# Kernel tuning notes

Measured on AMD Instinct MI355X. Metric: run time of the kernel, lower is better.

Reference implementation:

```python
import jax, jax.numpy as jnp
import numpy as np

HEADS = 6
EPS = 1e-5


def _na_idx(L, k, d):
    # NATTEN-style dilated neighborhood: work within dilation cosets,
    # clamp window to stay inside the image (window shifts at borders).
    i = np.arange(L)
    g = i % d
    p = i // d
    Lg = (L - g + d - 1) // d  # coset length per position
    start = np.clip(p - k // 2, 0, Lg - k)
    j = np.arange(k)
    nbr = g[:, None] + d * (start[:, None] + j[None, :])          # [L,k] neighbor coords
    rel = (start[:, None] + j[None, :]) - p[:, None] + (k - 1)    # [L,k] rpb index in [0,2k-2]
    return jnp.asarray(nbr, jnp.int32), jnp.asarray(rel, jnp.int32)


def _na2d(x, qkv_w, qkv_b, proj_w, proj_b, rpb, heads, k, d):
    # x: [B,H,W,C] NHWC neighborhood attention with relative positional bias
    B, H, W, C = x.shape
    dh = C // heads
    scale = dh ** -0.5
    qkv = (x @ qkv_w + qkv_b).reshape(B, H, W, 3, heads, dh)
    qkv = jnp.transpose(qkv, (3, 0, 4, 1, 2, 5))  # [3,B,h,H,W,dh]
    q, kk, v = qkv[0] * scale, qkv[1], qkv[2]
    nh, rh = _na_idx(H, k, d)
    nw, rw = _na_idx(W, k, d)

    def gather(t):  # [B,h,H,W,dh] -> [B,h,H,W,k,k,dh]
        t = t[:, :, nh]              # [B,h,H,k,W,dh]
        t = t[:, :, :, :, nw]        # [B,h,H,k,W,k,dh]
        return jnp.transpose(t, (0, 1, 2, 4, 3, 5, 6))

    kn, vn = gather(kk), gather(v)
    attn = jnp.einsum('bhxyd,bhxyijd->bhxyij', q, kn)  # [B,h,H,W,k,k]
    bias = rpb[:, rh]                  # [h,H,k,2k-1]
    bias = bias[:, :, :, rw]           # [h,H,k,W,k]
    bias = jnp.transpose(bias, (0, 1, 3, 2, 4))  # [h,H,W,k,k]
    attn = attn + bias[None]
    attn = jax.nn.softmax(attn.reshape(B, heads, H, W, k * k), axis=-1)
    attn = attn.reshape(B, heads, H, W, k, k)
    out = jnp.einsum('bhxyij,bhxyijd->bhxyd', attn, vn)
    out = jnp.transpose(out, (0, 2, 3, 1, 4)).reshape(B, H, W, C)
    return out @ proj_w + proj_b


def _rln(x, w, b, m1_w, m1_b, m2_w, m2_b):
    # Revised LayerNorm: normalize over (C,H,W) per sample; meta1/meta2 are 1x1 convs on std/mean
    mean = jnp.mean(x, axis=(1, 2, 3), keepdims=True)
    std = jnp.sqrt(jnp.mean((x - mean) ** 2, axis=(1, 2, 3), keepdims=True) + EPS)
    out = (x - mean) / std * w + b
    rescale = m1_w[None, :, None, None] * std + m1_b[None, :, None, None]
    rebias = m2_w[None, :, None, None] * mean + m2_b[None, :, None, None]
    return out, rescale, rebias


def _c11(x, w, b):  # 1x1 conv on NCHW == per-pixel linear
    return jnp.einsum('bchw,oc->bohw', x, w) + b[None, :, None, None]


def _gelu(x):
    return jax.nn.gelu(x, approximate=False)


def reference(x, ln_w, ln_b, m1_w, m1_b, m2_w, m2_b, qkv1_w, qkv1_b, proj1_w, proj1_b, rpb1, qkv2_w, qkv2_b, proj2_w, proj2_b, rpb2, mlp_w1, mlp_b1, mlp_w2, mlp_b2, bn_g, bn_b, bn_m, bn_v, pa_w1, pa_b1, pa_w2, pa_b2, ca_w1, ca_b1, ca_w2, ca_b2, m2a_w1, m2a_b1, m2a_w2, m2a_b2):
    # ---- NA block 1 (kernel 7, dilation 1) ----
    sc = x
    y, rs, rb = _rln(x, ln_w, ln_b, m1_w, m1_b, m2_w, m2_b)
    a = _na2d(jnp.transpose(y, (0, 2, 3, 1)), qkv1_w, qkv1_b, proj1_w, proj1_b, rpb1, HEADS, 7, 1)
    x = sc + jnp.transpose(a, (0, 3, 1, 2)) * rs + rb
    # ---- NA block 2 (kernel 5, dilation 8) ----
    sc = x
    y, rs, rb = _rln(x, ln_w, ln_b, m1_w, m1_b, m2_w, m2_b)
    a = _na2d(jnp.transpose(y, (0, 2, 3, 1)), qkv2_w, qkv2_b, proj2_w, proj2_b, rpb2, HEADS, 5, 8)
    x = sc + jnp.transpose(a, (0, 3, 1, 2)) * rs + rb
    # ---- MLP (source reuses the pre-attn2 shortcut `sc`) ----
    y, rs, rb = _rln(x, ln_w, ln_b, m1_w, m1_b, m2_w, m2_b)
    m = _c11(jax.nn.relu(_c11(y, mlp_w1, mlp_b1)), mlp_w2, mlp_b2)
    x = sc + m * rs + rb
    # ---- BN + pixel attention + channel attention + mlp2 ----
    sc = x
    inv = jax.lax.rsqrt(bn_v + EPS)
    y = (x - bn_m[None, :, None, None]) * (inv * bn_g)[None, :, None, None] + bn_b[None, :, None, None]
    pa = jax.nn.sigmoid(_c11(_gelu(_c11(y, pa_w1, pa_b1)), pa_w2, pa_b2))  # [B,1,H,W]
    y = pa * y
    gap = jnp.mean(y, axis=(2, 3), keepdims=True)
    ca = jax.nn.sigmoid(_c11(_gelu(_c11(gap, ca_w1, ca_b1)), ca_w2, ca_b2))  # [B,C,1,1]
    y = ca * y
    y = _c11(_gelu(_c11(y, m2a_w1, m2a_b1)), m2a_w2, m2a_b2)
    return sc + y


def setup_inputs() -> dict:
    key = jax.random.key(0)
    B, C, H, W, HID = 4, 96, 64, 64, 384
    ks = iter(jax.random.split(key, 48))

    def rn(shape, s=0.02):
        return jax.random.normal(next(ks), shape, jnp.float32) * s

    d = {}
    d['x'] = jax.random.normal(next(ks), (B, C, H, W), jnp.float32)
    d['ln_w'] = jnp.ones((1, C, 1, 1), jnp.float32)
    d['ln_b'] = jnp.zeros((1, C, 1, 1), jnp.float32)
    d['m1_w'] = rn((C,)); d['m1_b'] = jnp.ones((C,), jnp.float32)
    d['m2_w'] = rn((C,)); d['m2_b'] = jnp.zeros((C,), jnp.float32)
    d['qkv1_w'] = rn((C, 3 * C)); d['qkv1_b'] = jnp.zeros((3 * C,), jnp.float32)
    d['proj1_w'] = rn((C, C)); d['proj1_b'] = jnp.zeros((C,), jnp.float32)
    d['rpb1'] = rn((HEADS, 13, 13))
    d['qkv2_w'] = rn((C, 3 * C)); d['qkv2_b'] = jnp.zeros((3 * C,), jnp.float32)
    d['proj2_w'] = rn((C, C)); d['proj2_b'] = jnp.zeros((C,), jnp.float32)
    d['rpb2'] = rn((HEADS, 9, 9))
    d['mlp_w1'] = rn((HID, C)); d['mlp_b1'] = jnp.zeros((HID,), jnp.float32)
    d['mlp_w2'] = rn((C, HID)); d['mlp_b2'] = jnp.zeros((C,), jnp.float32)
    d['bn_g'] = jnp.ones((C,), jnp.float32); d['bn_b'] = jnp.zeros((C,), jnp.float32)
    d['bn_m'] = jnp.zeros((C,), jnp.float32); d['bn_v'] = jnp.ones((C,), jnp.float32)
    d['pa_w1'] = rn((C // 8, C)); d['pa_b1'] = jnp.zeros((C // 8,), jnp.float32)
    d['pa_w2'] = rn((1, C // 8)); d['pa_b2'] = jnp.zeros((1,), jnp.float32)
    d['ca_w1'] = rn((C, C)); d['ca_b1'] = jnp.zeros((C,), jnp.float32)
    d['ca_w2'] = rn((C, C)); d['ca_b2'] = jnp.zeros((C,), jnp.float32)
    d['m2a_w1'] = rn((C, C)); d['m2a_b1'] = jnp.zeros((C,), jnp.float32)
    d['m2a_w2'] = rn((C, C)); d['m2a_b2'] = jnp.zeros((C,), jnp.float32)
    return d
```

## Files before the change

### kernel.cpp

```cpp
#include <hip/hip_runtime.h>
#include <math.h>

#define CC 96
#define NP 4096
#define NHEADS 6
#define NELEMF 393216.0f
#define EPSF 1e-5f

typedef __attribute__((ext_vector_type(8))) short bf16x8;
typedef __attribute__((ext_vector_type(4))) float f32x4;
#define MFMA16(a,b,c) __builtin_amdgcn_mfma_f32_16x16x32_bf16(a,b,c,0,0,0)

#define WQKV1  64
#define WQKV2  (WQKV1+13824)
#define WPROJ1 (WQKV2+13824)
#define WPROJ2 (WPROJ1+4608)
#define WMLP1  (WPROJ2+4608)
#define WMLP2  (WMLP1+18432)
#define WM2A1  (WMLP2+18432)
#define WM2A2  (WM2A1+4608)
#define WPA1T  (WM2A2+4608)
#define WBNS   (WPA1T+1152)
#define WCA1T  (WBNS+192)
#define WCA2T  (WCA1T+9216)
#define WS_Q   870784
#define WS_K   (WS_Q+786432)
#define WS_V   (WS_K+786432)
#define WS_ATTPM (WS_V+786432)
#define WS_X1  (WS_ATTPM+786432)
#define WS_X2  (WS_X1+1572864)
#define WS_X3  (WS_X2+1572864)
#define WS_PA  (WS_X3+1572864)
#define WS_GAP (WS_PA+16384)

__device__ __forceinline__ float gelu_f(float x){
  return 0.5f * x * (1.0f + erff(x * 0.7071067811865476f));
}
__device__ __forceinline__ float sigmoid_f(float x){
  return 1.0f / (1.0f + __expf(-x));
}
__device__ __forceinline__ unsigned short bfr(float f){
  unsigned int u = __float_as_uint(f);
  u += 0x7fffu + ((u >> 16) & 1u);
  return (unsigned short)(u >> 16);
}
__device__ __forceinline__ float bflo16(unsigned short u){ return __uint_as_float(((unsigned int)u) << 16); }
__device__ __forceinline__ float bflo(unsigned int u){ return __uint_as_float(u << 16); }
__device__ __forceinline__ float bfhi(unsigned int u){ return __uint_as_float(u & 0xffff0000u); }
__device__ __forceinline__ void get_ms(const float* st, int b, float& mean, float& inv, float& stdv){
  float s = st[b], s2 = st[4+b];
  mean = s * (1.0f/NELEMF);
  float var = fmaxf(s2 * (1.0f/NELEMF) - mean*mean, 0.0f);
  stdv = sqrtf(var + EPSF);
  inv = 1.0f / stdv;
}
__device__ __forceinline__ float ldf(const float* p, int i){ return p[i]; }
__device__ __forceinline__ float ldf(const unsigned short* p, int i){ return bflo16(p[i]); }
__device__ __forceinline__ void load4(const float* p, float4& v){ v = *(const float4*)p; }
__device__ __forceinline__ void load4(const unsigned short* p, float4& v){
  ushort4 u = *(const ushort4*)p;
  v.x = bflo16(u.x); v.y = bflo16(u.y); v.z = bflo16(u.z); v.w = bflo16(u.w);
}

__device__ __forceinline__ float dotg(const float* qv, const uint4* p){
  uint4 a = p[0], b = p[1];
  float s;
  s  = qv[0]*bflo(a.x);            s = fmaf(qv[1],  bfhi(a.x), s);
  s = fmaf(qv[2],  bflo(a.y), s);  s = fmaf(qv[3],  bfhi(a.y), s);
  s = fmaf(qv[4],  bflo(a.z), s);  s = fmaf(qv[5],  bfhi(a.z), s);
  s = fmaf(qv[6],  bflo(a.w), s);  s = fmaf(qv[7],  bfhi(a.w), s);
  s = fmaf(qv[8],  bflo(b.x), s);  s = fmaf(qv[9],  bfhi(b.x), s);
  s = fmaf(qv[10], bflo(b.y), s);  s = fmaf(qv[11], bfhi(b.y), s);
  s = fmaf(qv[12], bflo(b.z), s);  s = fmaf(qv[13], bfhi(b.z), s);
  s = fmaf(qv[14], bflo(b.w), s);  s = fmaf(qv[15], bfhi(b.w), s);
  return s;
}
__device__ __forceinline__ void pvg(float w, const uint4* p, float* acc){
  uint4 a = p[0], b = p[1];
  acc[0]  = fmaf(w, bflo(a.x), acc[0]);  acc[1]  = fmaf(w, bfhi(a.x), acc[1]);
  acc[2]  = fmaf(w, bflo(a.y), acc[2]);  acc[3]  = fmaf(w, bfhi(a.y), acc[3]);
  acc[4]  = fmaf(w, bflo(a.z), acc[4]);  acc[5]  = fmaf(w, bfhi(a.z), acc[5]);
  acc[6]  = fmaf(w, bflo(a.w), acc[6]);  acc[7]  = fmaf(w, bfhi(a.w), acc[7]);
  acc[8]  = fmaf(w, bflo(b.x), acc[8]);  acc[9]  = fmaf(w, bfhi(b.x), acc[9]);
  acc[10] = fmaf(w, bflo(b.y), acc[10]); acc[11] = fmaf(w, bfhi(b.y), acc[11]);
  acc[12] = fmaf(w, bflo(b.z), acc[12]); acc[13] = fmaf(w, bfhi(b.z), acc[13]);
  acc[14] = fmaf(w, bflo(b.w), acc[14]); acc[15] = fmaf(w, bfhi(b.w), acc[15]);
}

__global__ void prep_stats_kernel(const float* __restrict__ x, float* __restrict__ st,
                             const float* __restrict__ q1, const float* __restrict__ q2,
                             const float* __restrict__ p1, const float* __restrict__ p2,
                             const float* __restrict__ w1, const float* __restrict__ w2,
                             const float* __restrict__ a1, const float* __restrict__ a2,
                             const float* __restrict__ pw1,
                             const float* __restrict__ bg, const float* __restrict__ bb,
                             const float* __restrict__ bm, const float* __restrict__ bv,
                             const float* __restrict__ cw1, const float* __restrict__ cw2,
                             float* __restrict__ ws){
  if(blockIdx.x < 384){
    int b = blockIdx.x / CC, c = blockIdx.x % CC;
    const float4* p4 = (const float4*)(x + (size_t)(b*CC + c)*NP);
    float s = 0.f, s2 = 0.f;
    for(int i = threadIdx.x; i < 1024; i += 256){
      float4 v = p4[i];
      s += v.x + v.y + v.z + v.w;
      s2 = fmaf(v.x, v.x, fmaf(v.y, v.y, fmaf(v.z, v.z, fmaf(v.w, v.w, s2))));
    }
    for(int off = 32; off > 0; off >>= 1){ s += __shfl_down(s, off); s2 += __shfl_down(s2, off); }
    __shared__ float ls[8];
    int wid = threadIdx.x >> 6;
    if((threadIdx.x & 63) == 0){ ls[wid] = s; ls[4+wid] = s2; }
    __syncthreads();
    if(threadIdx.x == 0){
      atomicAdd(&st[b],   ls[0]+ls[1]+ls[2]+ls[3]);
      atomicAdd(&st[4+b], ls[4]+ls[5]+ls[6]+ls[7]);
    }
    return;
  }
  int gid = (blockIdx.x - 384)*256 + threadIdx.x;
  if(gid < 27648){ int n = gid/96, c = gid%96; ((unsigned short*)(ws+WQKV1))[gid] = bfr(q1[c*288+n]); }
  else if(gid < 55296){ int g = gid-27648; int n = g/96, c = g%96; ((unsigned short*)(ws+WQKV2))[g] = bfr(q2[c*288+n]); }
  else if(gid < 64512){ int g = gid-55296; int n = g/96, c = g%96; ((unsigned short*)(ws+WPROJ1))[g] = bfr(p1[c*96+n]); }
  else if(gid < 73728){ int g = gid-64512; int n = g/96, c = g%96; ((unsigned short*)(ws+WPROJ2))[g] = bfr(p2[c*96+n]); }
  else if(gid < 110592){ int g = gid-73728; ((unsigned short*)(ws+WMLP1))[g] = bfr(w1[g]); }
  else if(gid < 147456){ int g = gid-110592; ((unsigned short*)(ws+WMLP2))[g] = bfr(w2[g]); }
  else if(gid < 156672){ int g = gid-147456; ((unsigned short*)(ws+WM2A1))[g] = bfr(a1[g]); }
  else if(gid < 165888){ int g = gid-156672; ((unsigned short*)(ws+WM2A2))[g] = bfr(a2[g]); }
  else if(gid < 167040){ int g = gid-165888; int c = g/12, h = g%12; ws[WPA1T + g] = pw1[h*96+c]; }
  else if(gid < 167136){ int c = gid-167040;
    float sc = rsqrtf(bv[c] + EPSF) * bg[c];
    ws[WBNS + c] = sc;
    ws[WBNS + 96 + c] = bb[c] - bm[c]*sc;
  }
  else if(gid < 167520){ ws[WS_GAP + (gid-167136)] = 0.f; }
  else if(gid < 176736){ int g = gid-167520; int o = g/96, c = g%96; ws[WCA1T + c*96 + o] = cw1[g]; }
  else if(gid < 185952){ int g = gid-176736; int o = g/96, c = g%96; ws[WCA2T + c*96 + o] = cw2[g]; }
}

template<typename AT>
__global__ void __launch_bounds__(512) gemm_qkv_kernel(
    const AT* __restrict__ xin, const float* __restrict__ st,
    const float* __restrict__ lnw, const float* __restrict__ lnb,
    const unsigned short* __restrict__ wT, const float* __restrict__ qb,
    unsigned short* __restrict__ qo, unsigned short* __restrict__ ko, unsigned short* __restrict__ vo){
  __shared__ unsigned short Atl[64*104];
  __shared__ float scl[96], ofs[96];
  int m_base = blockIdx.x*64;
  int b = m_base >> 12, pxl0 = m_base & 4095;
  float mean, inv, stdv; get_ms(st, b, mean, inv, stdv);
  int tid = threadIdx.x;
  if(tid < 96){ float s = inv*lnw[tid]; scl[tid] = s; ofs[tid] = lnb[tid] - mean*s; }
  __syncthreads();
  const AT* src = xin + (size_t)b*CC*NP + pxl0;
  for(int idx = tid; idx < 96*16; idx += 512){
    int c = idx >> 4, p4 = (idx & 15) << 2;
    float4 v; load4(src + (size_t)c*NP + p4, v);
    float s = scl[c], o = ofs[c];
    Atl[(p4+0)*104 + c] = bfr(fmaf(v.x, s, o));
    Atl[(p4+1)*104 + c] = bfr(fmaf(v.y, s, o));
    Atl[(p4+2)*104 + c] = bfr(fmaf(v.z, s, o));
    Atl[(p4+3)*104 + c] = bfr(fmaf(v.w, s, o));
  }
  __syncthreads();
  int w = tid >> 6, lane = tid & 63, ml = lane & 15, q = lane >> 4;
  int row = w & 3, nh = w >> 2;
  const unsigned short* arow = Atl + (row*16 + ml)*104;
  bf16x8 av[3];
  #pragma unroll
  for(int ks = 0; ks < 3; ++ks) av[ks] = *(const bf16x8*)(arow + ks*32 + q*8);
  f32x4 z = {0.f,0.f,0.f,0.f};
  #pragma unroll
  for(int g0 = 0; g0 < 3; ++g0){
    int g = nh*3 + g0;
    f32x4 acc[3] = {z, z, z};
    #pragma unroll
    for(int ks = 0; ks < 3; ++ks){
      #pragma unroll
      for(int gg = 0; gg < 3; ++gg){
        bf16x8 bv = *(const bf16x8*)(wT + (g*48 + gg*16 + ml)*96 + ks*32 + q*8);
        acc[gg] = MFMA16(av[ks], bv, acc[gg]);
      }
    }
    #pragma unroll
    for(int gg = 0; gg < 3; ++gg){
      int nfb = g*48 + gg*16;
      int t = nfb/96, head = (nfb%96) >> 4;
      float scale = (t == 0) ? 0.25f : 1.0f;
      unsigned short* dst = (t == 0) ? qo : (t == 1) ? ko : vo;
      float bias = qb[nfb + ml];
      #pragma unroll
      for(int r = 0; r < 4; ++r){
        int pxl = pxl0 + row*16 + q*4 + r;
        dst[(((size_t)(b*NHEADS + head))*NP + pxl)*16 + ml] = bfr((acc[gg][r] + bias)*scale);
      }
    }
  }
}

template<int K, int D, int RPB, typename SCT>
__global__ void __launch_bounds__(512) attnproj_kernel(
    const unsigned short* __restrict__ qb, const unsigned short* __restrict__ kb,
    const unsigned short* __restrict__ vb, const float* __restrict__ rpb,
    const unsigned short* __restrict__ wT, const float* __restrict__ pb,
    const SCT* __restrict__ scx, const float* __restrict__ st,
    const float* __restrict__ m1w, const float* __restrict__ m1b,
    const float* __restrict__ m2w, const float* __restrict__ m2b,
    unsigned short* __restrict__ dst, float* __restrict__ st_out){
  __shared__ __align__(16) char smbuf[26624];
  __shared__ float rpbl[NHEADS*RPB*RPB];
  __shared__ float ls[16];
  unsigned short* attout = (unsigned short*)smbuf;
  float* T = (float*)smbuf;
  int b = blockIdx.x >> 6;
  int x = blockIdx.x & 63;
  int tid = threadIdx.x;
  for(int i = tid; i < NHEADS*RPB*RPB; i += 512) rpbl[i] = rpb[i];
  __syncthreads();

  if(tid < 384){
    int head = tid >> 6;
    int y = tid & 63;
    int bh = b*NHEADS + head;
    int gx = (D == 1) ? 0 : (x & (D-1));
    int px = (D == 1) ? x : (x >> 3);
    int Lgx = (64 - gx + D - 1) / D;
    int sx = min(max(px - K/2, 0), Lgx - K);
    int gy = (D == 1) ? 0 : (y & (D-1));
    int py = (D == 1) ? y : (y >> 3);
    int Lgy = (64 - gy + D - 1) / D;
    int sy = min(max(py - K/2, 0), Lgy - K);
    int dxb = sx - px + (K-1);
    int dyb = sy - py + (K-1);
    int pix = x*64 + y;

    float qv[16];
    {
      const uint4* qg = (const uint4*)(qb + ((size_t)bh*NP + pix)*16);
      uint4 qa = qg[0], qb4 = qg[1];
      qv[0]=bflo(qa.x);  qv[1]=bfhi(qa.x);  qv[2]=bflo(qa.y);  qv[3]=bfhi(qa.y);
      qv[4]=bflo(qa.z);  qv[5]=bfhi(qa.z);  qv[6]=bflo(qa.w);  qv[7]=bfhi(qa.w);
      qv[8]=bflo(qb4.x); qv[9]=bfhi(qb4.x); qv[10]=bflo(qb4.y);qv[11]=bfhi(qb4.y);
      qv[12]=bflo(qb4.z);qv[13]=bfhi(qb4.z);qv[14]=bflo(qb4.w);qv[15]=bfhi(qb4.w);
    }
    const unsigned short* kgb = kb + (size_t)bh*NP*16;
    const unsigned short* vgb = vb + (size_t)bh*NP*16;

    float sc[K*K];
    #pragma unroll
    for(int i = 0; i < K; ++i){
      int colx = gx + D*(sx + i);
      const unsigned short* kcol = kgb + (size_t)colx*64*16;
      const float* br = rpbl + (head*RPB + (i + dxb))*RPB + dyb;
      #pragma unroll
      for(int j = 0; j < K; ++j){
        int wwy = gy + D*(sy + j);
        sc[i*K + j] = dotg(qv, (const uint4*)(kcol + wwy*16)) + br[j];
      }
    }
    float mx = -1e30f;
    #pragma unroll
    for(int n = 0; n < K*K; ++n) mx = fmaxf(mx, sc[n]);
    float sum = 0.f;
    #pragma unroll
    for(int n = 0; n < K*K; ++n){ float e = __expf(sc[n] - mx); sc[n] = e; sum += e; }
    float rs = 1.0f / sum;
    float acc[16];
    #pragma unroll
    for(int d = 0; d < 16; ++d) acc[d] = 0.f;
    #pragma unroll
    for(int i = 0; i < K; ++i){
      int colx = gx + D*(sx + i);
      const unsigned short* vcol = vgb + (size_t)colx*64*16;
      #pragma unroll
      for(int j = 0; j < K; ++j){
        int wwy = gy + D*(sy + j);
        pvg(sc[i*K + j] * rs, (const uint4*)(vcol + wwy*16), acc);
      }
    }
    unsigned int ow[8];
    #pragma unroll
    for(int p = 0; p < 8; ++p)
      ow[p] = (unsigned int)bfr(acc[2*p]) | ((unsigned int)bfr(acc[2*p+1]) << 16);
    unsigned short* op = attout + y*104 + head*16;
    *(uint4*)op = make_uint4(ow[0], ow[1], ow[2], ow[3]);
    *(uint4*)(op + 8) = make_uint4(ow[4], ow[5], ow[6], ow[7]);
  }
  __syncthreads();

  int w = tid >> 6, lane = tid & 63, ml = lane & 15, q = lane >> 4;
  int row = w & 3, nh = w >> 2;
  f32x4 z = {0.f,0.f,0.f,0.f};
  f32x4 acc[3] = {z, z, z};
  {
    const unsigned short* arow = attout + (row*16 + ml)*104;
    #pragma unroll
    for(int ks = 0; ks < 3; ++ks){
      bf16x8 av = *(const bf16x8*)(arow + ks*32 + q*8);
      #pragma unroll
      for(int g0 = 0; g0 < 3; ++g0){
        int g = nh*3 + g0;
        bf16x8 bv = *(const bf16x8*)(wT + (g*16 + ml)*96 + ks*32 + q*8);
        acc[g0] = MFMA16(av, bv, acc[g0]);
      }
    }
  }
  __syncthreads();
  #pragma unroll
  for(int g0 = 0; g0 < 3; ++g0){
    int g = nh*3 + g0;
    #pragma unroll
    for(int r = 0; r < 4; ++r)
      T[(g*16 + ml)*68 + row*16 + q*4 + r] = acc[g0][r];
  }
  __syncthreads();
  int pxl0 = x*64;
  float mean, inv, stdv; get_ms(st, b, mean, inv, stdv);
  float s = 0.f, s2 = 0.f;
  for(int idx = tid; idx < 96*64; idx += 512){
    int n = idx >> 6, p = idx & 63;
    float rsf = fmaf(m1w[n], stdv, m1b[n]);
    float rbf = fmaf(m2w[n], mean, m2b[n]);
    int ad = (b*CC + n)*NP + pxl0 + p;
    float val = ldf(scx, ad) + (T[n*68 + p] + pb[n])*rsf + rbf;
    dst[ad] = bfr(val);
    s += val; s2 = fmaf(val, val, s2);
  }
  for(int off = 32; off > 0; off >>= 1){ s += __shfl_down(s, off); s2 += __shfl_down(s2, off); }
  if(lane == 0){ ls[w] = s; ls[8+w] = s2; }
  __syncthreads();
  if(tid == 0){
    float a0 = 0.f, a1 = 0.f;
    #pragma unroll
    for(int i = 0; i < 8; ++i){ a0 += ls[i]; a1 += ls[8+i]; }
    atomicAdd(&st_out[b], a0);
    atomicAdd(&st_out[4+b], a1);
  }
}

__global__ void __launch_bounds__(512) gemm_mlp_kernel(
    const unsigned short* __restrict__ xin, const float* __restrict__ st,
    const float* __restrict__ lnw, const float* __restrict__ lnb,
    const unsigned short* __restrict__ w1T, const float* __restrict__ b1,
    const unsigned short* __restrict__ w2T, const float* __restrict__ b2,
    const unsigned short* __restrict__ scx,
    const float* __restrict__ m1w, const float* __restrict__ m1b,
    const float* __restrict__ m2w, const float* __restrict__ m2b,
    float* __restrict__ dst,
    const float* __restrict__ bns, const float* __restrict__ pw1t,
    const float* __restrict__ pb1, const float* __restrict__ pw2,
    const float* __restrict__ pb2, float* __restrict__ pa,
    float* __restrict__ gap){
  __shared__ __align__(16) char smbuf[63488];
  __shared__ float scl[96], ofs[96];
  unsigned short* Atl  = (unsigned short*)smbuf;
  unsigned short* hidL = (unsigned short*)(smbuf + 13312);
  float* T = (float*)(smbuf + 13312);
  float* gpart = (float*)smbuf;
  int m_base = blockIdx.x*64;
  int b = m_base >> 12, pxl0 = m_base & 4095;
  float mean, inv, stdv; get_ms(st, b, mean, inv, stdv);
  int tid = threadIdx.x;
  if(tid < 96){ float s = inv*lnw[tid]; scl[tid] = s; ofs[tid] = lnb[tid] - mean*s; }
  __syncthreads();
  const unsigned short* src = xin + (size_t)b*CC*NP + pxl0;
  for(int idx = tid; idx < 96*16; idx += 512){
    int c = idx >> 4, p4 = (idx & 15) << 2;
    float4 v; load4(src + (size_t)c*NP + p4, v);
    float s = scl[c], o = ofs[c];
    Atl[(p4+0)*104 + c] = bfr(fmaf(v.x, s, o));
    Atl[(p4+1)*104 + c] = bfr(fmaf(v.y, s, o));
    Atl[(p4+2)*104 + c] = bfr(fmaf(v.z, s, o));
    Atl[(p4+3)*104 + c] = bfr(fmaf(v.w, s, o));
  }
  __syncthreads();
  int w = tid >> 6, lane = tid & 63, ml = lane & 15, q = lane >> 4;
  int row = w & 3, nh = w >> 2;
  f32x4 z = {0.f,0.f,0.f,0.f};
  {
    const unsigned short* arow = Atl + (row*16 + ml)*104;
    bf16x8 av[3];
    #pragma unroll
    for(int ks = 0; ks < 3; ++ks) av[ks] = *(const bf16x8*)(arow + ks*32 + q*8);
    #pragma unroll
    for(int g0 = 0; g0 < 4; ++g0){
      int g = nh*4 + g0;
      f32x4 acc[3] = {z, z, z};
      #pragma unroll
      for(int ks = 0; ks < 3; ++ks){
        #pragma unroll
        for(int gg = 0; gg < 3; ++gg){
          bf16x8 bv = *(const bf16x8*)(w1T + (g*48 + gg*16 + ml)*96 + ks*32 + q*8);
          acc[gg] = MFMA16(av[ks], bv, acc[gg]);
        }
      }
      #pragma unroll
      for(int gg = 0; gg < 3; ++gg){
        int n = g*48 + gg*16 + ml;
        float bias = b1[n];
        #pragma unroll
        for(int r = 0; r < 4; ++r)
          hidL[(row*16 + q*4 + r)*392 + n] = bfr(fmaxf(acc[gg][r] + bias, 0.f));
      }
    }
  }
  __syncthreads();
  f32x4 acc2[3] = {z, z, z};
  {
    const unsigned short* arow = hidL + (row*16 + ml)*392;
    #pragma unroll
    for(int ks = 0; ks < 12; ++ks){
      bf16x8 av = *(const bf16x8*)(arow + ks*32 + q*8);
      #pragma unroll
      for(int g0 = 0; g0 < 3; ++g0){
        int g = nh*3 + g0;
        bf16x8 bv = *(const bf16x8*)(w2T + (g*16 + ml)*384 + ks*32 + q*8);
        acc2[g0] = MFMA16(av, bv, acc2[g0]);
      }
    }
  }
  __syncthreads();
  #pragma unroll
  for(int g0 = 0; g0 < 3; ++g0){
    int g = nh*3 + g0;
    #pragma unroll
    for(int r = 0; r < 4; ++r)
      T[(g*16 + ml)*68 + row*16 + q*4 + r] = acc2[g0][r];
  }
  __syncthreads();
  for(int idx = tid; idx < 96*64; idx += 512){
    int n = idx >> 6, px = idx & 63;
    float rsf = fmaf(m1w[n], stdv, m1b[n]);
    float rbf = fmaf(m2w[n], mean, m2b[n]);
    int ad = (b*CC + n)*NP + pxl0 + px;
    float val = ldf(scx, ad) + (T[n*68 + px] + b2[n])*rsf + rbf;
    dst[ad] = val;
    T[n*68 + px] = val;
  }
  __syncthreads();
  int pxq = tid >> 3, t = tid & 7;
  float yvv[12], acc[12];
  #pragma unroll
  for(int h = 0; h < 12; ++h) acc[h] = 0.f;
  #pragma unroll 6
  for(int cc = 0; cc < 12; ++cc){
    int c = t*12 + cc;
    float yv = fmaf(T[c*68 + pxq], bns[c], bns[96 + c]);
    yvv[cc] = yv;
    #pragma unroll
    for(int h = 0; h < 12; ++h) acc[h] = fmaf(yv, pw1t[c*12 + h], acc[h]);
  }
  #pragma unroll
  for(int h = 0; h < 12; ++h){
    acc[h] += __shfl_xor(acc[h], 1);
    acc[h] += __shfl_xor(acc[h], 2);
    acc[h] += __shfl_xor(acc[h], 4);
  }
  float s = pb2[0];
  #pragma unroll
  for(int h = 0; h < 12; ++h) s = fmaf(gelu_f(acc[h] + pb1[h]), pw2[h], s);
  float pav = sigmoid_f(s);
  if(t == 0) pa[b*NP + pxl0 + pxq] = pav;
  #pragma unroll 6
  for(int cc = 0; cc < 12; ++cc){
    float g = yvv[cc] * pav;
    g += __shfl_xor(g, 8);  g += __shfl_xor(g, 16); g += __shfl_xor(g, 32);
    if(lane < 8) gpart[w*96 + lane*12 + cc] = g;
  }
  __syncthreads();
  if(tid < 96){
    int c = tid;
    float v = 0.f;
    #pragma unroll
    for(int ww = 0; ww < 8; ++ww) v += gpart[ww*96 + c];
    atomicAdd(&gap[b*96 + c], v * (1.0f/4096.0f));
  }
}

__global__ void __launch_bounds__(512) gemm_m2a_kernel(
    const float* __restrict__ x3, const float* __restrict__ bns,
    const float* __restrict__ pa, const float* __restrict__ gap,
    const float* __restrict__ cw1T, const float* __restrict__ cb1,
    const float* __restrict__ cw2T, const float* __restrict__ cb2,
    const unsigned short* __restrict__ w1T, const float* __restrict__ b1,
    const unsigned short* __restrict__ w2T, const float* __restrict__ b2,
    const float* __restrict__ scx, float* __restrict__ outp){
  __shared__ __align__(16) char smbuf[26624];
  __shared__ float scl[96], ofs[96], pal[64];
  __shared__ float gl[96], tl[96];
  unsigned short* Atl = (unsigned short*)smbuf;
  unsigned short* tl2 = (unsigned short*)(smbuf + 13312);
  float* T = (float*)smbuf;
  int m_base = blockIdx.x*64;
  int b = m_base >> 12, pxl0 = m_base & 4095;
  int tid = threadIdx.x;
  if(tid < 96) gl[tid] = gap[b*96 + tid];
  if(tid >= 128 && tid < 192) pal[tid-128] = pa[m_base + (tid-128)];
  __syncthreads();
  if(tid < 96){
    float a = cb1[tid];
    #pragma unroll 8
    for(int c = 0; c < 96; ++c) a = fmaf(gl[c], cw1T[c*96 + tid], a);
    tl[tid] = gelu_f(a);
  }
  __syncthreads();
  if(tid < 96){
    float a = cb2[tid];
    #pragma unroll 8
    for(int c = 0; c < 96; ++c) a = fmaf(tl[c], cw2T[c*96 + tid], a);
    float cv = sigmoid_f(a);
    scl[tid] = bns[tid]*cv; ofs[tid] = bns[96+tid]*cv;
  }
  __syncthreads();
  const float* src = x3 + (size_t)b*CC*NP + pxl0;
  for(int idx = tid; idx < 96*16; idx += 512){
    int c = idx >> 4, p4 = (idx & 15) << 2;
    float4 v = *(const float4*)(src + (size_t)c*NP + p4);
    float s = scl[c], o = ofs[c];
    Atl[(p4+0)*104 + c] = bfr(fmaf(v.x, s, o) * pal[p4+0]);
    Atl[(p4+1)*104 + c] = bfr(fmaf(v.y, s, o) * pal[p4+1]);
    Atl[(p4+2)*104 + c] = bfr(fmaf(v.z, s, o) * pal[p4+2]);
    Atl[(p4+3)*104 + c] = bfr(fmaf(v.w, s, o) * pal[p4+3]);
  }
  __syncthreads();
  int w = tid >> 6, lane = tid & 63, ml = lane & 15, q = lane >> 4;
  int row = w & 3, nh = w >> 2;
  f32x4 z = {0.f,0.f,0.f,0.f};
  f32x4 acc1[3] = {z, z, z};
  {
    const unsigned short* arow = Atl + (row*16 + ml)*104;
    #pragma unroll
    for(int ks = 0; ks < 3; ++ks){
      bf16x8 av = *(const bf16x8*)(arow + ks*32 + q*8);
      #pragma unroll
      for(int g0 = 0; g0 < 3; ++g0){
        int g = nh*3 + g0;
        bf16x8 bv = *(const bf16x8*)(w1T + (g*16 + ml)*96 + ks*32 + q*8);
        acc1[g0] = MFMA16(av, bv, acc1[g0]);
      }
    }
  }
  #pragma unroll
  for(int g0 = 0; g0 < 3; ++g0){
    int g = nh*3 + g0;
    float bias = b1[g*16 + ml];
    #pragma unroll
    for(int r = 0; r < 4; ++r)
      tl2[(row*16 + q*4 + r)*104 + g*16 + ml] = bfr(gelu_f(acc1[g0][r] + bias));
  }
  __syncthreads();
  f32x4 acc2[3] = {z, z, z};
  {
    const unsigned short* arow = tl2 + (row*16 + ml)*104;
    #pragma unroll
    for(int ks = 0; ks < 3; ++ks){
      bf16x8 av = *(const bf16x8*)(arow + ks*32 + q*8);
      #pragma unroll
      for(int g0 = 0; g0 < 3; ++g0){
        int g = nh*3 + g0;
        bf16x8 bv = *(const bf16x8*)(w2T + (g*16 + ml)*96 + ks*32 + q*8);
        acc2[g0] = MFMA16(av, bv, acc2[g0]);
      }
    }
  }
  __syncthreads();
  #pragma unroll
  for(int g0 = 0; g0 < 3; ++g0){
    int g = nh*3 + g0;
    #pragma unroll
    for(int r = 0; r < 4; ++r)
      T[(g*16 + ml)*68 + row*16 + q*4 + r] = acc2[g0][r];
  }
  __syncthreads();
  for(int idx = tid; idx < 96*64; idx += 512){
    int n = idx >> 6, p = idx & 63;
    int ad = (b*CC + n)*NP + pxl0 + p;
    outp[ad] = scx[ad] + T[n*68 + p] + b2[n];
  }
}

extern "C" void kernel_launch(void* const* d_in, const int* in_sizes, int n_in,
                              void* d_out, int out_size, void* d_ws, size_t ws_size,
                              hipStream_t stream){
  (void)in_sizes; (void)n_in; (void)out_size; (void)ws_size;
  const float* x     = (const float*)d_in[0];
  const float* lnw   = (const float*)d_in[1];
  const float* lnb   = (const float*)d_in[2];
  const float* m1w   = (const float*)d_in[3];
  const float* m1b   = (const float*)d_in[4];
  const float* m2w   = (const float*)d_in[5];
  const float* m2b   = (const float*)d_in[6];
  const float* qkv1w = (const float*)d_in[7];
  const float* qkv1b = (const float*)d_in[8];
  const float* proj1w= (const float*)d_in[9];
  const float* proj1b= (const float*)d_in[10];
  const float* rpb1  = (const float*)d_in[11];
  const float* qkv2w = (const float*)d_in[12];
  const float* qkv2b = (const float*)d_in[13];
  const float* proj2w= (const float*)d_in[14];
  const float* proj2b= (const float*)d_in[15];
  const float* rpb2  = (const float*)d_in[16];
  const float* mw1   = (const float*)d_in[17];
  const float* mb1   = (const float*)d_in[18];
  const float* mw2   = (const float*)d_in[19];
  const float* mb2   = (const float*)d_in[20];
  const float* bng   = (const float*)d_in[21];
  const float* bnb   = (const float*)d_in[22];
  const float* bnm   = (const float*)d_in[23];
  const float* bnv   = (const float*)d_in[24];
  const float* paw1  = (const float*)d_in[25];
  const float* pab1  = (const float*)d_in[26];
  const float* paw2  = (const float*)d_in[27];
  const float* pab2  = (const float*)d_in[28];
  const float* caw1  = (const float*)d_in[29];
  const float* cab1  = (const float*)d_in[30];
  const float* caw2  = (const float*)d_in[31];
  const float* cab2  = (const float*)d_in[32];
  const float* aw1   = (const float*)d_in[33];
  const float* ab1   = (const float*)d_in[34];
  const float* aw2   = (const float*)d_in[35];
  const float* ab2   = (const float*)d_in[36];

  float* ws  = (float*)d_ws;
  float* out = (float*)d_out;
  float* st0 = ws;
  float* st1 = ws + 8;
  float* st2 = ws + 16;
  unsigned short* q     = (unsigned short*)(ws + WS_Q);
  unsigned short* k     = (unsigned short*)(ws + WS_K);
  unsigned short* v     = (unsigned short*)(ws + WS_V);
  unsigned short* x1b   = (unsigned short*)(ws + WS_X1);
  unsigned short* x2b   = (unsigned short*)(ws + WS_X2);
  float* x3  = ws + WS_X3;
  float* pab = ws + WS_PA;
  float* gpb = ws + WS_GAP;
  float* bns = ws + WBNS;

  hipMemsetAsync(d_ws, 0, 64*sizeof(float), stream);
  prep_stats_kernel<<<1111, 256, 0, stream>>>(x, st0, qkv1w, qkv2w, proj1w, proj2w,
                                              mw1, mw2, aw1, aw2, paw1,
                                              bng, bnb, bnm, bnv, caw1, caw2, ws);

  gemm_qkv_kernel<float><<<256, 512, 0, stream>>>(x, st0, lnw, lnb,
      (unsigned short*)(ws+WQKV1), qkv1b, q, k, v);
  attnproj_kernel<7,1,13,float><<<256, 512, 0, stream>>>(q, k, v, rpb1,
      (unsigned short*)(ws+WPROJ1), proj1b, x, st0, m1w, m1b, m2w, m2b, x1b, st1);

  gemm_qkv_kernel<unsigned short><<<256, 512, 0, stream>>>(x1b, st1, lnw, lnb,
      (unsigned short*)(ws+WQKV2), qkv2b, q, k, v);
  attnproj_kernel<5,8,9,unsigned short><<<256, 512, 0, stream>>>(q, k, v, rpb2,
      (unsigned short*)(ws+WPROJ2), proj2b, x1b, st1, m1w, m1b, m2w, m2b, x2b, st2);

  gemm_mlp_kernel<<<256, 512, 0, stream>>>(x2b, st2, lnw, lnb,
      (unsigned short*)(ws+WMLP1), mb1, (unsigned short*)(ws+WMLP2), mb2,
      x1b, m1w, m1b, m2w, m2b, x3,
      bns, ws + WPA1T, pab1, paw2, pab2, pab, gpb);

  gemm_m2a_kernel<<<256, 512, 0, stream>>>(x3, bns, pab, gpb,
                                           ws + WCA1T, cab1, ws + WCA2T, cab2,
                                           (unsigned short*)(ws+WM2A1), ab1,
                                           (unsigned short*)(ws+WM2A2), ab2, x3, out);
}
```

Before: 251.0 us.

## Double block size to 1024 threads, split attention neighborhood across thread pairs

All main kernels now launch 1024 threads per block instead of 512, with the per-wave work in the GEMM stages redistributed across 16 waves. The neighborhood attention stage splits each query's window rows between two threads and combines the max, sum and output accumulators with lane shuffles, which halves per-thread register demand and serial latency. Block indices are also swizzled so that neighbouring workgroups map to spread-out tiles. The aim is more latency hiding in the memory-bound gather loops, at the cost of uneven wave work (some waves get one output tile, others two) and extra shuffles.

Result: slower. 326.6 us (+30.1%).

```diff
diff --git a/kernel.cpp b/kernel.cpp
--- a/kernel.cpp
+++ b/kernel.cpp
@@ -26,8 +26,7 @@
 #define WS_Q   870784
 #define WS_K   (WS_Q+786432)
 #define WS_V   (WS_K+786432)
-#define WS_ATTPM (WS_V+786432)
-#define WS_X1  (WS_ATTPM+786432)
+#define WS_X1  (WS_V+786432+786432)
 #define WS_X2  (WS_X1+1572864)
 #define WS_X3  (WS_X2+1572864)
 #define WS_PA  (WS_X3+1572864)
@@ -61,7 +60,6 @@
   ushort4 u = *(const ushort4*)p;
   v.x = bflo16(u.x); v.y = bflo16(u.y); v.z = bflo16(u.z); v.w = bflo16(u.w);
 }
-
 __device__ __forceinline__ float dotg(const float* qv, const uint4* p){
   uint4 a = p[0], b = p[1];
   float s;
@@ -85,6 +83,53 @@
   acc[10] = fmaf(w, bflo(b.y), acc[10]); acc[11] = fmaf(w, bfhi(b.y), acc[11]);
   acc[12] = fmaf(w, bflo(b.z), acc[12]); acc[13] = fmaf(w, bfhi(b.z), acc[13]);
   acc[14] = fmaf(w, bflo(b.w), acc[14]); acc[15] = fmaf(w, bfhi(b.w), acc[15]);
+}
+__device__ __forceinline__ int xswz(int bid){ return ((bid & 7) << 5) | (bid >> 3); }
+
+template<int NI, int K, int D>
+__device__ __forceinline__ float attn_scores(
+    int i0, const float* qv, const unsigned short* kgb,
+    int gx, int sx, int gy, int sy,
+    const float* br0, int rpb_stride, float* sc){
+  float mx = -1e30f;
+  #pragma unroll
+  for(int ii = 0; ii < NI; ++ii){
+    int i = i0 + ii;
+    int colx = gx + D*(sx + i);
+    const unsigned short* kcol = kgb + (size_t)colx*64*16;
+    const float* br = br0 + i*rpb_stride;
+    #pragma unroll
+    for(int j = 0; j < K; ++j){
+      int wwy = gy + D*(sy + j);
+      float s = dotg(qv, (const uint4*)(kcol + wwy*16)) + br[j];
+      sc[ii*K + j] = s;
+      mx = fmaxf(mx, s);
+    }
+  }
+  return mx;
+}
+template<int NI, int K>
+__device__ __forceinline__ float attn_expsum(float* sc, float mx){
+  float sum = 0.f;
+  #pragma unroll
+  for(int n = 0; n < NI*K; ++n){ float e = __expf(sc[n] - mx); sc[n] = e; sum += e; }
+  return sum;
+}
+template<int NI, int K, int D>
+__device__ __forceinline__ void attn_pv(
+    int i0, const float* sc, float rs, const unsigned short* vgb,
+    int gx, int sx, int gy, int sy, float* acc){
+  #pragma unroll
+  for(int ii = 0; ii < NI; ++ii){
+    int i = i0 + ii;
+    int colx = gx + D*(sx + i);
+    const unsigned short* vcol = vgb + (size_t)colx*64*16;
+    #pragma unroll
+    for(int j = 0; j < K; ++j){
+      int wwy = gy + D*(sy + j);
+      pvg(sc[ii*K + j] * rs, (const uint4*)(vcol + wwy*16), acc);
+    }
+  }
 }
 
 __global__ void prep_stats_kernel(const float* __restrict__ x, float* __restrict__ st,
@@ -138,21 +183,22 @@
 }
 
 template<typename AT>
-__global__ void __launch_bounds__(512) gemm_qkv_kernel(
+__global__ void __launch_bounds__(1024) gemm_qkv_kernel(
     const AT* __restrict__ xin, const float* __restrict__ st,
     const float* __restrict__ lnw, const float* __restrict__ lnb,
     const unsigned short* __restrict__ wT, const float* __restrict__ qb,
     unsigned short* __restrict__ qo, unsigned short* __restrict__ ko, unsigned short* __restrict__ vo){
   __shared__ unsigned short Atl[64*104];
   __shared__ float scl[96], ofs[96];
-  int m_base = blockIdx.x*64;
+  int wid = xswz(blockIdx.x);
+  int m_base = wid*64;
   int b = m_base >> 12, pxl0 = m_base & 4095;
   float mean, inv, stdv; get_ms(st, b, mean, inv, stdv);
   int tid = threadIdx.x;
   if(tid < 96){ float s = inv*lnw[tid]; scl[tid] = s; ofs[tid] = lnb[tid] - mean*s; }
   __syncthreads();
   const AT* src = xin + (size_t)b*CC*NP + pxl0;
-  for(int idx = tid; idx < 96*16; idx += 512){
+  for(int idx = tid; idx < 96*16; idx += 1024){
     int c = idx >> 4, p4 = (idx & 15) << 2;
     float4 v; load4(src + (size_t)c*NP + p4, v);
     float s = scl[c], o = ofs[c];
@@ -169,36 +215,28 @@
   #pragma unroll
   for(int ks = 0; ks < 3; ++ks) av[ks] = *(const bf16x8*)(arow + ks*32 + q*8);
   f32x4 z = {0.f,0.f,0.f,0.f};
-  #pragma unroll
-  for(int g0 = 0; g0 < 3; ++g0){
-    int g = nh*3 + g0;
-    f32x4 acc[3] = {z, z, z};
+  for(int g = nh; g < 18; g += 4){
+    f32x4 acc = z;
     #pragma unroll
     for(int ks = 0; ks < 3; ++ks){
-      #pragma unroll
-      for(int gg = 0; gg < 3; ++gg){
-        bf16x8 bv = *(const bf16x8*)(wT + (g*48 + gg*16 + ml)*96 + ks*32 + q*8);
-        acc[gg] = MFMA16(av[ks], bv, acc[gg]);
-      }
-    }
-    #pragma unroll
-    for(int gg = 0; gg < 3; ++gg){
-      int nfb = g*48 + gg*16;
-      int t = nfb/96, head = (nfb%96) >> 4;
-      float scale = (t == 0) ? 0.25f : 1.0f;
-      unsigned short* dst = (t == 0) ? qo : (t == 1) ? ko : vo;
-      float bias = qb[nfb + ml];
-      #pragma unroll
-      for(int r = 0; r < 4; ++r){
-        int pxl = pxl0 + row*16 + q*4 + r;
-        dst[(((size_t)(b*NHEADS + head))*NP + pxl)*16 + ml] = bfr((acc[gg][r] + bias)*scale);
-      }
+      bf16x8 bv = *(const bf16x8*)(wT + (g*16 + ml)*96 + ks*32 + q*8);
+      acc = MFMA16(av[ks], bv, acc);
+    }
+    int nfb = g*16;
+    int t = nfb/96, head = (nfb%96) >> 4;
+    float scale = (t == 0) ? 0.25f : 1.0f;
+    unsigned short* dst = (t == 0) ? qo : (t == 1) ? ko : vo;
+    float bias = qb[nfb + ml];
+    #pragma unroll
+    for(int r = 0; r < 4; ++r){
+      int pxl = pxl0 + row*16 + q*4 + r;
+      dst[(((size_t)(b*NHEADS + head))*NP + pxl)*16 + ml] = bfr((acc[r] + bias)*scale);
     }
   }
 }
 
 template<int K, int D, int RPB, typename SCT>
-__global__ void __launch_bounds__(512) attnproj_kernel(
+__global__ void __launch_bounds__(1024) attnproj_kernel(
     const unsigned short* __restrict__ qb, const unsigned short* __restrict__ kb,
     const unsigned short* __restrict__ vb, const float* __restrict__ rpb,
     const unsigned short* __restrict__ wT, const float* __restrict__ pb,
@@ -208,18 +246,23 @@
     unsigned short* __restrict__ dst, float* __restrict__ st_out){
   __shared__ __align__(16) char smbuf[26624];
   __shared__ float rpbl[NHEADS*RPB*RPB];
-  __shared__ float ls[16];
+  __shared__ float ls[32];
   unsigned short* attout = (unsigned short*)smbuf;
   float* T = (float*)smbuf;
-  int b = blockIdx.x >> 6;
-  int x = blockIdx.x & 63;
+  int wid = xswz(blockIdx.x);
+  int b = wid >> 6;
+  int x = wid & 63;
   int tid = threadIdx.x;
-  for(int i = tid; i < NHEADS*RPB*RPB; i += 512) rpbl[i] = rpb[i];
-  __syncthreads();
-
-  if(tid < 384){
-    int head = tid >> 6;
-    int y = tid & 63;
+  for(int i = tid; i < NHEADS*RPB*RPB; i += 1024) rpbl[i] = rpb[i];
+  __syncthreads();
+
+  constexpr int KLO = (K+1)/2;
+  constexpr int KH2 = K - KLO;
+  if(tid < 768){
+    int half = tid & 1;
+    int hy = tid >> 1;
+    int head = hy >> 6;
+    int y = hy & 63;
     int bh = b*NHEADS + head;
     int gx = (D == 1) ? 0 : (x & (D-1));
     int px = (D == 1) ? x : (x >> 3);
@@ -244,79 +287,75 @@
     }
     const unsigned short* kgb = kb + (size_t)bh*NP*16;
     const unsigned short* vgb = vb + (size_t)bh*NP*16;
-
-    float sc[K*K];
-    #pragma unroll
-    for(int i = 0; i < K; ++i){
-      int colx = gx + D*(sx + i);
-      const unsigned short* kcol = kgb + (size_t)colx*64*16;
-      const float* br = rpbl + (head*RPB + (i + dxb))*RPB + dyb;
-      #pragma unroll
-      for(int j = 0; j < K; ++j){
-        int wwy = gy + D*(sy + j);
-        sc[i*K + j] = dotg(qv, (const uint4*)(kcol + wwy*16)) + br[j];
-      }
-    }
-    float mx = -1e30f;
-    #pragma unroll
-    for(int n = 0; n < K*K; ++n) mx = fmaxf(mx, sc[n]);
-    float sum = 0.f;
-    #pragma unroll
-    for(int n = 0; n < K*K; ++n){ float e = __expf(sc[n] - mx); sc[n] = e; sum += e; }
+    const float* br0 = rpbl + (head*RPB + dxb)*RPB + dyb;
+
+    float sc[KLO*K];
+    float mx;
+    if(half == 0) mx = attn_scores<KLO,K,D>(0,   qv, kgb, gx, sx, gy, sy, br0, RPB, sc);
+    else          mx = attn_scores<KH2,K,D>(KLO, qv, kgb, gx, sx, gy, sy, br0, RPB, sc);
+    mx = fmaxf(mx, __shfl_xor(mx, 1));
+    float sum;
+    if(half == 0) sum = attn_expsum<KLO,K>(sc, mx);
+    else          sum = attn_expsum<KH2,K>(sc, mx);
+    sum += __shfl_xor(sum, 1);
     float rs = 1.0f / sum;
     float acc[16];
     #pragma unroll
     for(int d = 0; d < 16; ++d) acc[d] = 0.f;
-    #pragma unroll
-    for(int i = 0; i < K; ++i){
-      int colx = gx + D*(sx + i);
-      const unsigned short* vcol = vgb + (size_t)colx*64*16;
+    if(half == 0) attn_pv<KLO,K,D>(0,   sc, rs, vgb, gx, sx, gy, sy, acc);
+    else          attn_pv<KH2,K,D>(KLO, sc, rs, vgb, gx, sx, gy, sy, acc);
+    #pragma unroll
+    for(int d = 0; d < 16; ++d) acc[d] += __shfl_xor(acc[d], 1);
+    if(half == 0){
+      unsigned int ow[8];
       #pragma unroll
-      for(int j = 0; j < K; ++j){
-        int wwy = gy + D*(sy + j);
-        pvg(sc[i*K + j] * rs, (const uint4*)(vcol + wwy*16), acc);
-      }
-    }
-    unsigned int ow[8];
-    #pragma unroll
-    for(int p = 0; p < 8; ++p)
-      ow[p] = (unsigned int)bfr(acc[2*p]) | ((unsigned int)bfr(acc[2*p+1]) << 16);
-    unsigned short* op = attout + y*104 + head*16;
-    *(uint4*)op = make_uint4(ow[0], ow[1], ow[2], ow[3]);
-    *(uint4*)(op + 8) = make_uint4(ow[4], ow[5], ow[6], ow[7]);
+      for(int p = 0; p < 8; ++p)
+        ow[p] = (unsigned int)bfr(acc[2*p]) | ((unsigned int)bfr(acc[2*p+1]) << 16);
+      unsigned short* op = attout + y*104 + head*16;
+      *(uint4*)op = make_uint4(ow[0], ow[1], ow[2], ow[3]);
+      *(uint4*)(op + 8) = make_uint4(ow[4], ow[5], ow[6], ow[7]);
+    }
   }
   __syncthreads();
 
   int w = tid >> 6, lane = tid & 63, ml = lane & 15, q = lane >> 4;
   int row = w & 3, nh = w >> 2;
+  int gA = nh, gB = nh + 4;
+  bool hasB = (gB < 6);
   f32x4 z = {0.f,0.f,0.f,0.f};
-  f32x4 acc[3] = {z, z, z};
+  f32x4 accA = z, accB = z;
   {
     const unsigned short* arow = attout + (row*16 + ml)*104;
+    bf16x8 av[3];
+    #pragma unroll
+    for(int ks = 0; ks < 3; ++ks) av[ks] = *(const bf16x8*)(arow + ks*32 + q*8);
     #pragma unroll
     for(int ks = 0; ks < 3; ++ks){
-      bf16x8 av = *(const bf16x8*)(arow + ks*32 + q*8);
+      bf16x8 bvA = *(const bf16x8*)(wT + (gA*16 + ml)*96 + ks*32 + q*8);
+      accA = MFMA16(av[ks], bvA, accA);
+    }
+    if(hasB){
       #pragma unroll
-      for(int g0 = 0; g0 < 3; ++g0){
-        int g = nh*3 + g0;
-        bf16x8 bv = *(const bf16x8*)(wT + (g*16 + ml)*96 + ks*32 + q*8);
-        acc[g0] = MFMA16(av, bv, acc[g0]);
+      for(int ks = 0; ks < 3; ++ks){
+        bf16x8 bvB = *(const bf16x8*)(wT + (gB*16 + ml)*96 + ks*32 + q*8);
+        accB = MFMA16(av[ks], bvB, accB);
       }
     }
   }
   __syncthreads();
   #pragma unroll
-  for(int g0 = 0; g0 < 3; ++g0){
-    int g = nh*3 + g0;
+  for(int r = 0; r < 4; ++r)
+    T[(gA*16 + ml)*68 + row*16 + q*4 + r] = accA[r];
+  if(hasB){
     #pragma unroll
     for(int r = 0; r < 4; ++r)
-      T[(g*16 + ml)*68 + row*16 + q*4 + r] = acc[g0][r];
+      T[(gB*16 + ml)*68 + row*16 + q*4 + r] = accB[r];
   }
   __syncthreads();
   int pxl0 = x*64;
   float mean, inv, stdv; get_ms(st, b, mean, inv, stdv);
   float s = 0.f, s2 = 0.f;
-  for(int idx = tid; idx < 96*64; idx += 512){
+  for(int idx = tid; idx < 96*64; idx += 1024){
     int n = idx >> 6, p = idx & 63;
     float rsf = fmaf(m1w[n], stdv, m1b[n]);
     float rbf = fmaf(m2w[n], mean, m2b[n]);
@@ -326,18 +365,18 @@
     s += val; s2 = fmaf(val, val, s2);
   }
   for(int off = 32; off > 0; off >>= 1){ s += __shfl_down(s, off); s2 += __shfl_down(s2, off); }
-  if(lane == 0){ ls[w] = s; ls[8+w] = s2; }
+  if(lane == 0){ ls[w] = s; ls[16+w] = s2; }
   __syncthreads();
   if(tid == 0){
     float a0 = 0.f, a1 = 0.f;
     #pragma unroll
-    for(int i = 0; i < 8; ++i){ a0 += ls[i]; a1 += ls[8+i]; }
+    for(int i = 0; i < 16; ++i){ a0 += ls[i]; a1 += ls[16+i]; }
     atomicAdd(&st_out[b], a0);
     atomicAdd(&st_out[4+b], a1);
   }
 }
 
-__global__ void __launch_bounds__(512) gemm_mlp_kernel(
+__global__ void __launch_bounds__(1024) gemm_mlp_kernel(
     const unsigned short* __restrict__ xin, const float* __restrict__ st,
     const float* __restrict__ lnw, const float* __restrict__ lnb,
     const unsigned short* __restrict__ w1T, const float* __restrict__ b1,
@@ -356,14 +395,15 @@
   unsigned short* hidL = (unsigned short*)(smbuf + 13312);
   float* T = (float*)(smbuf + 13312);
   float* gpart = (float*)smbuf;
-  int m_base = blockIdx.x*64;
+  int wid = xswz(blockIdx.x);
+  int m_base = wid*64;
   int b = m_base >> 12, pxl0 = m_base & 4095;
   float mean, inv, stdv; get_ms(st, b, mean, inv, stdv);
   int tid = threadIdx.x;
   if(tid < 96){ float s = inv*lnw[tid]; scl[tid] = s; ofs[tid] = lnb[tid] - mean*s; }
   __syncthreads();
   const unsigned short* src = xin + (size_t)b*CC*NP + pxl0;
-  for(int idx = tid; idx < 96*16; idx += 512){
+  for(int idx = tid; idx < 96*16; idx += 1024){
     int c = idx >> 4, p4 = (idx & 15) << 2;
     float4 v; load4(src + (size_t)c*NP + p4, v);
     float s = scl[c], o = ofs[c];
@@ -382,8 +422,8 @@
     #pragma unroll
     for(int ks = 0; ks < 3; ++ks) av[ks] = *(const bf16x8*)(arow + ks*32 + q*8);
     #pragma unroll
-    for(int g0 = 0; g0 < 4; ++g0){
-      int g = nh*4 + g0;
+    for(int g0 = 0; g0 < 2; ++g0){
+      int g = nh*2 + g0;
       f32x4 acc[3] = {z, z, z};
       #pragma unroll
       for(int ks = 0; ks < 3; ++ks){
@@ -404,30 +444,32 @@
     }
   }
   __syncthreads();
-  f32x4 acc2[3] = {z, z, z};
+  int gA = nh, gB = nh + 4;
+  bool hasB = (gB < 6);
+  f32x4 accA = z, accB = z;
   {
     const unsigned short* arow = hidL + (row*16 + ml)*392;
-    #pragma unroll
     for(int ks = 0; ks < 12; ++ks){
       bf16x8 av = *(const bf16x8*)(arow + ks*32 + q*8);
-      #pragma unroll
-      for(int g0 = 0; g0 < 3; ++g0){
-        int g = nh*3 + g0;
-        bf16x8 bv = *(const bf16x8*)(w2T + (g*16 + ml)*384 + ks*32 + q*8);
-        acc2[g0] = MFMA16(av, bv, acc2[g0]);
+      bf16x8 bvA = *(const bf16x8*)(w2T + (gA*16 + ml)*384 + ks*32 + q*8);
+      accA = MFMA16(av, bvA, accA);
+      if(hasB){
+        bf16x8 bvB = *(const bf16x8*)(w2T + (gB*16 + ml)*384 + ks*32 + q*8);
+        accB = MFMA16(av, bvB, accB);
       }
     }
   }
   __syncthreads();
   #pragma unroll
-  for(int g0 = 0; g0 < 3; ++g0){
-    int g = nh*3 + g0;
+  for(int r = 0; r < 4; ++r)
+    T[(gA*16 + ml)*68 + row*16 + q*4 + r] = accA[r];
+  if(hasB){
     #pragma unroll
     for(int r = 0; r < 4; ++r)
-      T[(g*16 + ml)*68 + row*16 + q*4 + r] = acc2[g0][r];
-  }
-  __syncthreads();
-  for(int idx = tid; idx < 96*64; idx += 512){
+      T[(gB*16 + ml)*68 + row*16 + q*4 + r] = accB[r];
+  }
+  __syncthreads();
+  for(int idx = tid; idx < 96*64; idx += 1024){
     int n = idx >> 6, px = idx & 63;
     float rsf = fmaf(m1w[n], stdv, m1b[n]);
     float rbf = fmaf(m2w[n], mean, m2b[n]);
@@ -437,34 +479,36 @@
     T[n*68 + px] = val;
   }
   __syncthreads();
-  int pxq = tid >> 3, t = tid & 7;
-  float yvv[12], acc[12];
-  #pragma unroll
-  for(int h = 0; h < 12; ++h) acc[h] = 0.f;
-  #pragma unroll 6
-  for(int cc = 0; cc < 12; ++cc){
-    int c = t*12 + cc;
-    float yv = fmaf(T[c*68 + pxq], bns[c], bns[96 + c]);
-    yvv[cc] = yv;
-    #pragma unroll
-    for(int h = 0; h < 12; ++h) acc[h] = fmaf(yv, pw1t[c*12 + h], acc[h]);
-  }
-  #pragma unroll
-  for(int h = 0; h < 12; ++h){
-    acc[h] += __shfl_xor(acc[h], 1);
-    acc[h] += __shfl_xor(acc[h], 2);
-    acc[h] += __shfl_xor(acc[h], 4);
-  }
-  float s = pb2[0];
-  #pragma unroll
-  for(int h = 0; h < 12; ++h) s = fmaf(gelu_f(acc[h] + pb1[h]), pw2[h], s);
-  float pav = sigmoid_f(s);
-  if(t == 0) pa[b*NP + pxl0 + pxq] = pav;
-  #pragma unroll 6
-  for(int cc = 0; cc < 12; ++cc){
-    float g = yvv[cc] * pav;
-    g += __shfl_xor(g, 8);  g += __shfl_xor(g, 16); g += __shfl_xor(g, 32);
-    if(lane < 8) gpart[w*96 + lane*12 + cc] = g;
+  if(tid < 512){
+    int pxq = tid >> 3, t = tid & 7;
+    float yvv[12], acc[12];
+    #pragma unroll
+    for(int h = 0; h < 12; ++h) acc[h] = 0.f;
+    #pragma unroll 6
+    for(int cc = 0; cc < 12; ++cc){
+      int c = t*12 + cc;
+      float yv = fmaf(T[c*68 + pxq], bns[c], bns[96 + c]);
+      yvv[cc] = yv;
+      #pragma unroll
+      for(int h = 0; h < 12; ++h) acc[h] = fmaf(yv, pw1t[c*12 + h], acc[h]);
+    }
+    #pragma unroll
+    for(int h = 0; h < 12; ++h){
+      acc[h] += __shfl_xor(acc[h], 1);
+      acc[h] += __shfl_xor(acc[h], 2);
+      acc[h] += __shfl_xor(acc[h], 4);
+    }
+    float s = pb2[0];
+    #pragma unroll
+    for(int h = 0; h < 12; ++h) s = fmaf(gelu_f(acc[h] + pb1[h]), pw2[h], s);
+    float pav = sigmoid_f(s);
+    if(t == 0) pa[b*NP + pxl0 + pxq] = pav;
+    #pragma unroll 6
+    for(int cc = 0; cc < 12; ++cc){
+      float g = yvv[cc] * pav;
+      g += __shfl_xor(g, 8);  g += __shfl_xor(g, 16); g += __shfl_xor(g, 32);
+      if(lane < 8) gpart[w*96 + lane*12 + cc] = g;
+    }
   }
   __syncthreads();
   if(tid < 96){
@@ -476,7 +520,7 @@
   }
 }
 
-__global__ void __launch_bounds__(512) gemm_m2a_kernel(
+__global__ void __launch_bounds__(1024) gemm_m2a_kernel(
     const float* __restrict__ x3, const float* __restrict__ bns,
     const float* __restrict__ pa, const float* __restrict__ gap,
     const float* __restrict__ cw1T, const float* __restrict__ cb1,
@@ -490,7 +534,8 @@
   unsigned short* Atl = (unsigned short*)smbuf;
   unsigned short* tl2 = (unsigned short*)(smbuf + 13312);
   float* T = (float*)smbuf;
-  int m_base = blockIdx.x*64;
+  int wid = xswz(blockIdx.x);
+  int m_base = wid*64;
   int b = m_base >> 12, pxl0 = m_base & 4095;
   int tid = threadIdx.x;
   if(tid < 96) gl[tid] = gap[b*96 + tid];
@@ -512,7 +557,7 @@
   }
   __syncthreads();
   const float* src = x3 + (size_t)b*CC*NP + pxl0;
-  for(int idx = tid; idx < 96*16; idx += 512){
+  for(int idx = tid; idx < 96*16; idx += 1024){
     int c = idx >> 4, p4 = (idx & 15) << 2;
     float4 v = *(const float4*)(src + (size_t)c*NP + p4);
     float s = scl[c], o = ofs[c];
@@ -525,53 +570,52 @@
   int w = tid >> 6, lane = tid & 63, ml = lane & 15, q = lane >> 4;
   int row = w & 3, nh = w >> 2;
   f32x4 z = {0.f,0.f,0.f,0.f};
-  f32x4 acc1[3] = {z, z, z};
   {
     const unsigned short* arow = Atl + (row*16 + ml)*104;
+    bf16x8 av[3];
+    #pragma unroll
+    for(int ks = 0; ks < 3; ++ks) av[ks] = *(const bf16x8*)(arow + ks*32 + q*8);
+    for(int g = nh; g < 6; g += 4){
+      f32x4 acc1 = z;
+      #pragma unroll
+      for(int ks = 0; ks < 3; ++ks){
+        bf16x8 bv = *(const bf16x8*)(w1T + (g*16 + ml)*96 + ks*32 + q*8);
+        acc1 = MFMA16(av[ks], bv, acc1);
+      }
+      float bias = b1[g*16 + ml];
+      #pragma unroll
+      for(int r = 0; r < 4; ++r)
+        tl2[(row*16 + q*4 + r)*104 + g*16 + ml] = bfr(gelu_f(acc1[r] + bias));
+    }
+  }
+  __syncthreads();
+  int gA = nh, gB = nh + 4;
+  bool hasB = (gB < 6);
+  f32x4 accA = z, accB = z;
+  {
+    const unsigned short* arow = tl2 + (row*16 + ml)*104;
     #pragma unroll
     for(int ks = 0; ks < 3; ++ks){
       bf16x8 av = *(const bf16x8*)(arow + ks*32 + q*8);
-      #pragma unroll
-      for(int g0 = 0; g0 < 3; ++g0){
-        int g = nh*3 + g0;
-        bf16x8 bv = *(const bf16x8*)(w1T + (g*16 + ml)*96 + ks*32 + q*8);
-        acc1[g0] = MFMA16(av, bv, acc1[g0]);
+      bf16x8 bvA = *(const bf16x8*)(w2T + (gA*16 + ml)*96 + ks*32 + q*8);
+      accA = MFMA16(av, bvA, accA);
+      if(hasB){
+        bf16x8 bvB = *(const bf16x8*)(w2T + (gB*16 + ml)*96 + ks*32 + q*8);
+        accB = MFMA16(av, bvB, accB);
       }
     }
   }
+  __syncthreads();
   #pragma unroll
-  for(int g0 = 0; g0 < 3; ++g0){
-    int g = nh*3 + g0;
-    float bias = b1[g*16 + ml];
+  for(int r = 0; r < 4; ++r)
+    T[(gA*16 + ml)*68 + row*16 + q*4 + r] = accA[r];
+  if(hasB){
     #pragma unroll
     for(int r = 0; r < 4; ++r)
-      tl2[(row*16 + q*4 + r)*104 + g*16 + ml] = bfr(gelu_f(acc1[g0][r] + bias));
-  }
-  __syncthreads();
-  f32x4 acc2[3] = {z, z, z};
-  {
-    const unsigned short* arow = tl2 + (row*16 + ml)*104;
-    #pragma unroll
-    for(int ks = 0; ks < 3; ++ks){
-      bf16x8 av = *(const bf16x8*)(arow + ks*32 + q*8);
-      #pragma unroll
-      for(int g0 = 0; g0 < 3; ++g0){
-        int g = nh*3 + g0;
-        bf16x8 bv = *(const bf16x8*)(w2T + (g*16 + ml)*96 + ks*32 + q*8);
-        acc2[g0] = MFMA16(av, bv, acc2[g0]);
-      }
-    }
-  }
-  __syncthreads();
-  #pragma unroll
-  for(int g0 = 0; g0 < 3; ++g0){
-    int g = nh*3 + g0;
-    #pragma unroll
-    for(int r = 0; r < 4; ++r)
-      T[(g*16 + ml)*68 + row*16 + q*4 + r] = acc2[g0][r];
-  }
-  __syncthreads();
-  for(int idx = tid; idx < 96*64; idx += 512){
+      T[(gB*16 + ml)*68 + row*16 + q*4 + r] = accB[r];
+  }
+  __syncthreads();
+  for(int idx = tid; idx < 96*64; idx += 1024){
     int n = idx >> 6, p = idx & 63;
     int ad = (b*CC + n)*NP + pxl0 + p;
     outp[ad] = scx[ad] + T[n*68 + p] + b2[n];
@@ -640,23 +684,23 @@
                                               mw1, mw2, aw1, aw2, paw1,
                                               bng, bnb, bnm, bnv, caw1, caw2, ws);
 
-  gemm_qkv_kernel<float><<<256, 512, 0, stream>>>(x, st0, lnw, lnb,
+  gemm_qkv_kernel<float><<<256, 1024, 0, stream>>>(x, st0, lnw, lnb,
       (unsigned short*)(ws+WQKV1), qkv1b, q, k, v);
-  attnproj_kernel<7,1,13,float><<<256, 512, 0, stream>>>(q, k, v, rpb1,
+  attnproj_kernel<7,1,13,float><<<256, 1024, 0, stream>>>(q, k, v, rpb1,
       (unsigned short*)(ws+WPROJ1), proj1b, x, st0, m1w, m1b, m2w, m2b, x1b, st1);
 
-  gemm_qkv_kernel<unsigned short><<<256, 512, 0, stream>>>(x1b, st1, lnw, lnb,
+  gemm_qkv_kernel<unsigned short><<<256, 1024, 0, stream>>>(x1b, st1, lnw, lnb,
       (unsigned short*)(ws+WQKV2), qkv2b, q, k, v);
-  attnproj_kernel<5,8,9,unsigned short><<<256, 512, 0, stream>>>(q, k, v, rpb2,
+  attnproj_kernel<5,8,9,unsigned short><<<256, 1024, 0, stream>>>(q, k, v, rpb2,
       (unsigned short*)(ws+WPROJ2), proj2b, x1b, st1, m1w, m1b, m2w, m2b, x2b, st2);
 
-  gemm_mlp_kernel<<<256, 512, 0, stream>>>(x2b, st2, lnw, lnb,
+  gemm_mlp_kernel<<<256, 1024, 0, stream>>>(x2b, st2, lnw, lnb,
       (unsigned short*)(ws+WMLP1), mb1, (unsigned short*)(ws+WMLP2), mb2,
       x1b, m1w, m1b, m2w, m2b, x3,
       bns, ws + WPA1T, pab1, paw2, pab2, pab, gpb);
 
-  gemm_m2a_kernel<<<256, 512, 0, stream>>>(x3, bns, pab, gpb,
-                                           ws + WCA1T, cab1, ws + WCA2T, cab2,
-                                           (unsigned short*)(ws+WM2A1), ab1,
-                                           (unsigned short*)(ws+WM2A2), ab2, x3, out);
-}
+  gemm_m2a_kernel<<<256, 1024, 0, stream>>>(x3, bns, pab, gpb,
+                                            ws + WCA1T, cab1, ws + WCA2T, cab2,
+                                            (unsigned short*)(ws+WM2A1), ab1,
+                                            (unsigned short*)(ws+WM2A2), ab2, x3, out);
+}
```
